# Optimization experiments

Measured on AMD Instinct MI355X. Metric: run time of the kernel, lower is better.

Reference implementation:

```python
import jax, jax.numpy as jnp
import numpy as np

B, S, J = 64, 16, 256
QDIM, IDIM, HDIM = 512, 512, 256


def setup_inputs() -> dict:
    key = jax.random.key(0)
    k1, k2, k3, k4, k5, k6 = jax.random.split(key, 6)
    query = jax.random.normal(k1, (B, QDIM), dtype=jnp.float32)
    other_semesters = jax.random.normal(k2, (B, S, J, IDIM), dtype=jnp.float32)
    mask = jax.random.randint(k3, (B, S, J), 0, 2).astype(bool)
    # nn.Linear(in, out, bias=False) weights have shape [out, in]
    sc_q = 1.0 / np.sqrt(QDIM)
    sc_i = 1.0 / np.sqrt(IDIM)
    Wq = jax.random.uniform(k4, (HDIM, QDIM), jnp.float32, -sc_q, sc_q)
    Wk = jax.random.uniform(k5, (HDIM, IDIM), jnp.float32, -sc_i, sc_i)
    Wv = jax.random.uniform(k6, (HDIM, IDIM), jnp.float32, -sc_i, sc_i)
    return {"query": query, "other_semesters": other_semesters, "mask": mask,
            "Wq": Wq, "Wk": Wk, "Wv": Wv}


def reference(query, other_semesters, mask, Wq, Wk, Wv):
    # Projections (Linear without bias: x @ W.T)
    Q = query @ Wq.T                                   # [b, h]
    K = jnp.einsum('bsji,hi->bsjh', other_semesters, Wk)  # [b, s, j, h]
    V = jnp.einsum('bsji,hi->bsjh', other_semesters, Wv)  # [b, s, j, h]
    scale = 1.0 / jnp.sqrt(jnp.float32(K.shape[-1]))
    scores = jnp.einsum('bh,bsjh->bsj', Q, K) * scale  # [b, s, j]
    scores = jnp.where(mask, -jnp.inf, scores)
    weights = jax.nn.softmax(scores, axis=-1)          # [b, s, j]
    out = jnp.einsum('bsj,bsjh->bsh', weights, V)      # [b, s, h]
    return out
```

## Files before the change

### kernel.cpp

```cpp
#include <hip/hip_runtime.h>
#include <hip/hip_bf16.h>
#include <math.h>


#define B_    64
#define S_    16
#define J_    256
#define QDIM_ 512
#define IDIM_ 512
#define HDIM_ 256

__global__ __launch_bounds__(256) void precompute_qk(
    const float* __restrict__ query, const float* __restrict__ Wq,
    const float* __restrict__ Wk, float* __restrict__ qk) {
  __shared__ float q_sh[QDIM_];
  __shared__ float Q_sh[HDIM_];
  const int b = blockIdx.x;
  const int t = threadIdx.x;

  q_sh[t]       = query[b * QDIM_ + t];
  q_sh[t + 256] = query[b * QDIM_ + t + 256];
  __syncthreads();

  float acc = 0.f;
  const float* wr = Wq + (size_t)t * QDIM_;
  #pragma unroll 4
  for (int q = 0; q < QDIM_; q += 4) {
    float4 w4 = *(const float4*)(wr + q);
    acc = fmaf(q_sh[q], w4.x, acc);
    acc = fmaf(q_sh[q + 1], w4.y, acc);
    acc = fmaf(q_sh[q + 2], w4.z, acc);
    acc = fmaf(q_sh[q + 3], w4.w, acc);
  }
  Q_sh[t] = acc;
  __syncthreads();

  const float scale = 0.0625f;
  float a0 = 0.f, a1 = 0.f;
  #pragma unroll 4
  for (int h = 0; h < HDIM_; ++h) {
    const float qh = Q_sh[h];
    a0 = fmaf(qh, Wk[(size_t)h * IDIM_ + t], a0);
    a1 = fmaf(qh, Wk[(size_t)h * IDIM_ + t + 256], a1);
  }
  qk[b * IDIM_ + t]       = a0 * scale;
  qk[b * IDIM_ + t + 256] = a1 * scale;
}

__global__ __launch_bounds__(256) void transpose_wv(
    const float* __restrict__ Wv, float* __restrict__ WvT) {
  __shared__ float tile[32][33];
  const int bx = blockIdx.x;
  const int by = blockIdx.y;
  const int tx = threadIdx.x & 31;
  const int ty = threadIdx.x >> 5;
  #pragma unroll
  for (int k = 0; k < 4; ++k) {
    const int h = by * 32 + ty + k * 8;
    tile[ty + k * 8][tx] = Wv[(size_t)h * IDIM_ + bx * 32 + tx];
  }
  __syncthreads();
  #pragma unroll
  for (int k = 0; k < 4; ++k) {
    const int i = bx * 32 + ty + k * 8;
    WvT[(size_t)i * HDIM_ + by * 32 + tx] = tile[tx][ty + k * 8];
  }
}

__global__ __launch_bounds__(256) void attn_pool(
    const float* __restrict__ x,
    const int* __restrict__ mask,
    const float* __restrict__ qk,
    const float* __restrict__ WvT,
    float* __restrict__ out) {
  __shared__ int   msk[J_];
  __shared__ float sm_m[4], sm_l[4];
  __shared__ float sm_pooled[4][IDIM_];
  __shared__ float sm_final[IDIM_];

  const int bs   = blockIdx.x;
  const int b    = bs >> 4;
  const int t    = threadIdx.x;
  const int w    = t >> 6;
  const int lane = t & 63;

  msk[t] = mask[bs * J_ + t];

  const float* qkb = qk + b * IDIM_;
  const float4 qk0 = *(const float4*)(qkb + lane * 4);
  const float4 qk1 = *(const float4*)(qkb + 256 + lane * 4);

  const float* xb = x + (size_t)bs * J_ * IDIM_;

  float  m = -INFINITY, l = 0.f;
  float4 p0 = {0.f, 0.f, 0.f, 0.f};
  float4 p1 = {0.f, 0.f, 0.f, 0.f};

  __syncthreads();

  const int j0 = w * 64;
  for (int jj = 0; jj < 64; ++jj) {
    const int j = j0 + jj;
    const float* xr = xb + (size_t)j * IDIM_;
    const float4 x0 = *(const float4*)(xr + lane * 4);
    const float4 x1 = *(const float4*)(xr + 256 + lane * 4);

    float part = x0.x * qk0.x + x0.y * qk0.y + x0.z * qk0.z + x0.w * qk0.w
               + x1.x * qk1.x + x1.y * qk1.y + x1.z * qk1.z + x1.w * qk1.w;
    #pragma unroll
    for (int d = 1; d < 64; d <<= 1) part += __shfl_xor(part, d, 64);

    if (!msk[j]) {
      const float nm    = fmaxf(m, part);
      const float alpha = __expf(m - nm);
      const float wgt   = __expf(part - nm);
      l = l * alpha + wgt;
      p0.x = fmaf(p0.x, alpha, wgt * x0.x);
      p0.y = fmaf(p0.y, alpha, wgt * x0.y);
      p0.z = fmaf(p0.z, alpha, wgt * x0.z);
      p0.w = fmaf(p0.w, alpha, wgt * x0.w);
      p1.x = fmaf(p1.x, alpha, wgt * x1.x);
      p1.y = fmaf(p1.y, alpha, wgt * x1.y);
      p1.z = fmaf(p1.z, alpha, wgt * x1.z);
      p1.w = fmaf(p1.w, alpha, wgt * x1.w);
      m = nm;
    }
  }

  if (lane == 0) { sm_m[w] = m; sm_l[w] = l; }
  *(float4*)&sm_pooled[w][lane * 4]       = p0;
  *(float4*)&sm_pooled[w][256 + lane * 4] = p1;
  __syncthreads();

  const float M  = fmaxf(fmaxf(sm_m[0], sm_m[1]), fmaxf(sm_m[2], sm_m[3]));
  const float c0 = __expf(sm_m[0] - M);
  const float c1 = __expf(sm_m[1] - M);
  const float c2 = __expf(sm_m[2] - M);
  const float c3 = __expf(sm_m[3] - M);
  const float L  = c0 * sm_l[0] + c1 * sm_l[1] + c2 * sm_l[2] + c3 * sm_l[3];
  const float invL = 1.0f / L;

  {
    const float v0 = c0 * sm_pooled[0][t] + c1 * sm_pooled[1][t]
                   + c2 * sm_pooled[2][t] + c3 * sm_pooled[3][t];
    const float v1 = c0 * sm_pooled[0][t + 256] + c1 * sm_pooled[1][t + 256]
                   + c2 * sm_pooled[2][t + 256] + c3 * sm_pooled[3][t + 256];
    sm_final[t]       = v0 * invL;
    sm_final[t + 256] = v1 * invL;
  }
  __syncthreads();

  float acc = 0.f;
  const float* wcol = WvT + t;
  #pragma unroll 8
  for (int i = 0; i < IDIM_; ++i) {
    acc = fmaf(sm_final[i], wcol[(size_t)i * HDIM_], acc);
  }
  out[(size_t)bs * HDIM_ + t] = acc;
}

extern "C" void kernel_launch(void* const* d_in, const int* in_sizes, int n_in,
                              void* d_out, int out_size, void* d_ws, size_t ws_size,
                              hipStream_t stream) {
  const float* query = (const float*)d_in[0];
  const float* x     = (const float*)d_in[1];
  const int*   mask  = (const int*)d_in[2];
  const float* Wq    = (const float*)d_in[3];
  const float* Wk    = (const float*)d_in[4];
  const float* Wv    = (const float*)d_in[5];
  float* out = (float*)d_out;

  float* qk  = (float*)d_ws;
  float* WvT = qk + B_ * IDIM_;

  precompute_qk<<<B_, 256, 0, stream>>>(query, Wq, Wk, qk);
  transpose_wv<<<dim3(IDIM_ / 32, HDIM_ / 32), 256, 0, stream>>>(Wv, WvT);
  attn_pool<<<B_ * S_, 256, 0, stream>>>(x, mask, qk, WvT, out);
}
```

Measured before the change: 751.7 us.

## Skip masked rows via ballot, drop online softmax max, merge prep kernels

In attn_pool, each wave builds a 64-bit ballot of its mask bits and skips masked rows entirely, so their x data is never loaded or reduced. The online-softmax running max and rescaling are removed; scores are exponentiated directly and the per-wave partial sums are added without correction factors. The two preprocessing kernels are merged into one 192-block launch to save a launch. Without max subtraction, exp can overflow if scores are large, so correctness relies on scores staying in a moderate range.

```diff
diff --git a/kernel.cpp b/kernel.cpp
--- a/kernel.cpp
+++ b/kernel.cpp
@@ -10,60 +10,63 @@
 #define IDIM_ 512
 #define HDIM_ 256
 
-__global__ __launch_bounds__(256) void precompute_qk(
+__global__ __launch_bounds__(256) void prep(
     const float* __restrict__ query, const float* __restrict__ Wq,
-    const float* __restrict__ Wk, float* __restrict__ qk) {
+    const float* __restrict__ Wk, const float* __restrict__ Wv,
+    float* __restrict__ qk, float* __restrict__ WvT) {
   __shared__ float q_sh[QDIM_];
   __shared__ float Q_sh[HDIM_];
-  const int b = blockIdx.x;
+  __shared__ float tile[32][33];
+
+  const int blk = blockIdx.x;
   const int t = threadIdx.x;
 
-  q_sh[t]       = query[b * QDIM_ + t];
-  q_sh[t + 256] = query[b * QDIM_ + t + 256];
-  __syncthreads();
+  if (blk < 64) {
+    const int b = blk;
+    q_sh[t]       = query[b * QDIM_ + t];
+    q_sh[t + 256] = query[b * QDIM_ + t + 256];
+    __syncthreads();
 
-  float acc = 0.f;
-  const float* wr = Wq + (size_t)t * QDIM_;
-  #pragma unroll 4
-  for (int q = 0; q < QDIM_; q += 4) {
-    float4 w4 = *(const float4*)(wr + q);
-    acc = fmaf(q_sh[q], w4.x, acc);
-    acc = fmaf(q_sh[q + 1], w4.y, acc);
-    acc = fmaf(q_sh[q + 2], w4.z, acc);
-    acc = fmaf(q_sh[q + 3], w4.w, acc);
-  }
-  Q_sh[t] = acc;
-  __syncthreads();
+    float acc = 0.f;
+    const float* wr = Wq + (size_t)t * QDIM_;
+    #pragma unroll 4
+    for (int q = 0; q < QDIM_; q += 4) {
+      float4 w4 = *(const float4*)(wr + q);
+      acc = fmaf(q_sh[q], w4.x, acc);
+      acc = fmaf(q_sh[q + 1], w4.y, acc);
+      acc = fmaf(q_sh[q + 2], w4.z, acc);
+      acc = fmaf(q_sh[q + 3], w4.w, acc);
+    }
+    Q_sh[t] = acc;
+    __syncthreads();
 
-  const float scale = 0.0625f;
-  float a0 = 0.f, a1 = 0.f;
-  #pragma unroll 4
-  for (int h = 0; h < HDIM_; ++h) {
-    const float qh = Q_sh[h];
-    a0 = fmaf(qh, Wk[(size_t)h * IDIM_ + t], a0);
-    a1 = fmaf(qh, Wk[(size_t)h * IDIM_ + t + 256], a1);
-  }
-  qk[b * IDIM_ + t]       = a0 * scale;
-  qk[b * IDIM_ + t + 256] = a1 * scale;
-}
-
-__global__ __launch_bounds__(256) void transpose_wv(
-    const float* __restrict__ Wv, float* __restrict__ WvT) {
-  __shared__ float tile[32][33];
-  const int bx = blockIdx.x;
-  const int by = blockIdx.y;
-  const int tx = threadIdx.x & 31;
-  const int ty = threadIdx.x >> 5;
-  #pragma unroll
-  for (int k = 0; k < 4; ++k) {
-    const int h = by * 32 + ty + k * 8;
-    tile[ty + k * 8][tx] = Wv[(size_t)h * IDIM_ + bx * 32 + tx];
-  }
-  __syncthreads();
-  #pragma unroll
-  for (int k = 0; k < 4; ++k) {
-    const int i = bx * 32 + ty + k * 8;
-    WvT[(size_t)i * HDIM_ + by * 32 + tx] = tile[tx][ty + k * 8];
+    const float scale = 0.0625f;
+    float a0 = 0.f, a1 = 0.f;
+    #pragma unroll 4
+    for (int h = 0; h < HDIM_; ++h) {
+      const float qh = Q_sh[h];
+      a0 = fmaf(qh, Wk[(size_t)h * IDIM_ + t], a0);
+      a1 = fmaf(qh, Wk[(size_t)h * IDIM_ + t + 256], a1);
+    }
+    qk[b * IDIM_ + t]       = a0 * scale;
+    qk[b * IDIM_ + t + 256] = a1 * scale;
+  } else {
+    const int k = blk - 64;
+    const int bx = k & 15;
+    const int by = k >> 4;
+    const int tx = t & 31;
+    const int ty = t >> 5;
+    #pragma unroll
+    for (int kk = 0; kk < 4; ++kk) {
+      const int h = by * 32 + ty + kk * 8;
+      tile[ty + kk * 8][tx] = Wv[(size_t)h * IDIM_ + bx * 32 + tx];
+    }
+    __syncthreads();
+    #pragma unroll
+    for (int kk = 0; kk < 4; ++kk) {
+      const int i = bx * 32 + ty + kk * 8;
+      WvT[(size_t)i * HDIM_ + by * 32 + tx] = tile[tx][ty + kk * 8];
+    }
   }
 }
 
@@ -74,7 +77,7 @@
     const float* __restrict__ WvT,
     float* __restrict__ out) {
   __shared__ int   msk[J_];
-  __shared__ float sm_m[4], sm_l[4];
+  __shared__ float sm_l[4];
   __shared__ float sm_pooled[4][IDIM_];
   __shared__ float sm_final[IDIM_];
 
@@ -90,18 +93,19 @@
   const float4 qk0 = *(const float4*)(qkb + lane * 4);
   const float4 qk1 = *(const float4*)(qkb + 256 + lane * 4);
 
-  const float* xb = x + (size_t)bs * J_ * IDIM_;
+  const float* xb = x + (size_t)bs * J_ * IDIM_ + (size_t)(w * 64) * IDIM_;
 
-  float  m = -INFINITY, l = 0.f;
+  float  l = 0.f;
   float4 p0 = {0.f, 0.f, 0.f, 0.f};
   float4 p1 = {0.f, 0.f, 0.f, 0.f};
 
   __syncthreads();
 
-  const int j0 = w * 64;
+  const unsigned long long mb = __ballot(msk[w * 64 + lane] != 0);
+
   for (int jj = 0; jj < 64; ++jj) {
-    const int j = j0 + jj;
-    const float* xr = xb + (size_t)j * IDIM_;
+    if ((mb >> jj) & 1ull) continue;
+    const float* xr = xb + (size_t)jj * IDIM_;
     const float4 x0 = *(const float4*)(xr + lane * 4);
     const float4 x1 = *(const float4*)(xr + 256 + lane * 4);
 
@@ -110,44 +114,30 @@
     #pragma unroll
     for (int d = 1; d < 64; d <<= 1) part += __shfl_xor(part, d, 64);
 
-    if (!msk[j]) {
-      const float nm    = fmaxf(m, part);
-      const float alpha = __expf(m - nm);
-      const float wgt   = __expf(part - nm);
-      l = l * alpha + wgt;
-      p0.x = fmaf(p0.x, alpha, wgt * x0.x);
-      p0.y = fmaf(p0.y, alpha, wgt * x0.y);
-      p0.z = fmaf(p0.z, alpha, wgt * x0.z);
-      p0.w = fmaf(p0.w, alpha, wgt * x0.w);
-      p1.x = fmaf(p1.x, alpha, wgt * x1.x);
-      p1.y = fmaf(p1.y, alpha, wgt * x1.y);
-      p1.z = fmaf(p1.z, alpha, wgt * x1.z);
-      p1.w = fmaf(p1.w, alpha, wgt * x1.w);
-      m = nm;
-    }
+    const float wgt = __expf(part);
+    l += wgt;
+    p0.x = fmaf(wgt, x0.x, p0.x);
+    p0.y = fmaf(wgt, x0.y, p0.y);
+    p0.z = fmaf(wgt, x0.z, p0.z);
+    p0.w = fmaf(wgt, x0.w, p0.w);
+    p1.x = fmaf(wgt, x1.x, p1.x);
+    p1.y = fmaf(wgt, x1.y, p1.y);
+    p1.z = fmaf(wgt, x1.z, p1.z);
+    p1.w = fmaf(wgt, x1.w, p1.w);
   }
 
-  if (lane == 0) { sm_m[w] = m; sm_l[w] = l; }
+  if (lane == 0) sm_l[w] = l;
   *(float4*)&sm_pooled[w][lane * 4]       = p0;
   *(float4*)&sm_pooled[w][256 + lane * 4] = p1;
   __syncthreads();
 
-  const float M  = fmaxf(fmaxf(sm_m[0], sm_m[1]), fmaxf(sm_m[2], sm_m[3]));
-  const float c0 = __expf(sm_m[0] - M);
-  const float c1 = __expf(sm_m[1] - M);
-  const float c2 = __expf(sm_m[2] - M);
-  const float c3 = __expf(sm_m[3] - M);
-  const float L  = c0 * sm_l[0] + c1 * sm_l[1] + c2 * sm_l[2] + c3 * sm_l[3];
+  const float L = sm_l[0] + sm_l[1] + sm_l[2] + sm_l[3];
   const float invL = 1.0f / L;
 
-  {
-    const float v0 = c0 * sm_pooled[0][t] + c1 * sm_pooled[1][t]
-                   + c2 * sm_pooled[2][t] + c3 * sm_pooled[3][t];
-    const float v1 = c0 * sm_pooled[0][t + 256] + c1 * sm_pooled[1][t + 256]
-                   + c2 * sm_pooled[2][t + 256] + c3 * sm_pooled[3][t + 256];
-    sm_final[t]       = v0 * invL;
-    sm_final[t + 256] = v1 * invL;
-  }
+  sm_final[t] = (sm_pooled[0][t] + sm_pooled[1][t] +
+                 sm_pooled[2][t] + sm_pooled[3][t]) * invL;
+  sm_final[t + 256] = (sm_pooled[0][t + 256] + sm_pooled[1][t + 256] +
+                       sm_pooled[2][t + 256] + sm_pooled[3][t + 256]) * invL;
   __syncthreads();
 
   float acc = 0.f;
@@ -173,7 +163,6 @@
   float* qk  = (float*)d_ws;
   float* WvT = qk + B_ * IDIM_;
 
-  precompute_qk<<<B_, 256, 0, stream>>>(query, Wq, Wk, qk);
-  transpose_wv<<<dim3(IDIM_ / 32, HDIM_ / 32), 256, 0, stream>>>(Wv, WvT);
+  prep<<<192, 256, 0, stream>>>(query, Wq, Wk, Wv, qk, WvT);
   attn_pool<<<B_ * S_, 256, 0, stream>>>(x, mask, qk, WvT, out);
 }
```

New measurement: 705.9 us. 1.06x faster.
